# Optimization experiments

Hardware: AMD Instinct MI355X
Metric: run time of the kernel (lower is better)

Reference implementation:

```python
import jax, jax.numpy as jnp
import numpy as np


def setup_inputs() -> dict:
    key = jax.random.key(0)
    k0, k1, k2, k3 = jax.random.split(key, 4)
    B, N, C = 4, 1024, 64
    x = jax.random.normal(k0, (B, N, C), dtype=jnp.float32)
    # torch nn.Linear weights are [out, in]; all projections are bias-free
    W1 = jax.random.normal(k1, (C, C), dtype=jnp.float32) * (1.0 / np.sqrt(C))
    W2 = jax.random.normal(k2, (C, C), dtype=jnp.float32) * (1.0 / np.sqrt(C))
    w3 = jax.random.normal(k3, (C,), dtype=jnp.float32) * (1.0 / np.sqrt(C))
    return {"x": x, "W1": W1, "W2": W2, "w3": w3}


def reference(x, W1, W2, w3):
    # x: [B, N, C]; torch Linear: y = x @ W.T
    x1 = jnp.einsum("bnc,dc->bnd", x, W1)  # [B, N, C]
    x2 = jnp.einsum("bnc,dc->bnd", x, W2)  # [B, N, C]
    # broadcast-add over node pairs, tanh, project C -> 1: [B, N, N]
    combined = jnp.tanh(x1[:, :, None, :] + x2[:, None, :, :])  # [B, N, N, C]
    att = jnp.einsum("bijc,c->bij", combined, w3)
    return jax.nn.softmax(att, axis=-1)
```

## Files before the change

kernel.cpp:

```cpp
#include <hip/hip_runtime.h>
#include <hip/hip_bf16.h>


#define BATCH 4
#define NN    1024
#define CC    64
#define TI    4
#define BLK   256
#define J2    2
#define NCH   (NN / (BLK * J2))
#define PP    65

__device__ __forceinline__ float fast_exp2(float x) {
#if __has_builtin(__builtin_amdgcn_exp2f)
    return __builtin_amdgcn_exp2f(x);
#else
    return exp2f(x);
#endif
}
__device__ __forceinline__ float fast_rcp(float x) {
#if __has_builtin(__builtin_amdgcn_rcpf)
    return __builtin_amdgcn_rcpf(x);
#else
    return 1.0f / x;
#endif
}

__global__ __launch_bounds__(256) void proj_kernel(
    const float* __restrict__ x, const float* __restrict__ W1,
    const float* __restrict__ W2, float* __restrict__ e1p,
    float* __restrict__ e2p) {
    __shared__ float w1t[CC * PP];
    __shared__ float w2t[CC * PP];

    const int tid = threadIdx.x;
    {
        const float4* __restrict__ W1v = (const float4*)W1;
        const float4* __restrict__ W2v = (const float4*)W2;
#pragma unroll
        for (int k = 0; k < 4; ++k) {
            const int fi = k * 256 + tid;
            const int r  = fi >> 4;
            const int c4 = (fi & 15) * 4;
            float4 a = W1v[fi], b = W2v[fi];
            w1t[(c4 + 0) * PP + r] = a.x; w1t[(c4 + 1) * PP + r] = a.y;
            w1t[(c4 + 2) * PP + r] = a.z; w1t[(c4 + 3) * PP + r] = a.w;
            w2t[(c4 + 0) * PP + r] = b.x; w2t[(c4 + 1) * PP + r] = b.y;
            w2t[(c4 + 2) * PP + r] = b.z; w2t[(c4 + 3) * PP + r] = b.w;
        }
    }
    __syncthreads();

    const int w    = tid >> 6;
    const int lane = tid & 63;
    const int r    = blockIdx.x * 4 + w;
    const float4* __restrict__ xr = (const float4*)(x + (size_t)r * CC);

    float a1 = 0.f, a2 = 0.f;
#pragma unroll
    for (int q = 0; q < 16; ++q) {
        const float4 xv = xr[q];
        const float xc[4] = {xv.x, xv.y, xv.z, xv.w};
#pragma unroll
        for (int m = 0; m < 4; ++m) {
            const int c = 4 * q + m;
            a1 = fmaf(xc[m], w1t[c * PP + lane], a1);
            a2 = fmaf(xc[m], w2t[c * PP + lane], a2);
        }
    }
    const float K2 = 2.8853900817779268f;
    e1p[(size_t)r * CC + lane] = fast_exp2(fminf(a1 * K2, 15.f));
    e2p[(size_t)r * CC + lane] = fast_exp2(fminf(a2 * K2, 15.f));
}

__device__ __forceinline__ void step2(float e1a, float e1b, float e2,
                                      float wc, float2& acc) {
    float da = fmaf(e1a, e2, 1.f);
    float db = fmaf(e1b, e2, 1.f);
    float r  = fast_rcp(da * db);
    acc.x = fmaf(wc * db, r, acc.x);
    acc.y = fmaf(wc * da, r, acc.y);
}

__global__ __launch_bounds__(BLK) void attn_kernel(
    const float* __restrict__ e1p, const float* __restrict__ e2p,
    const float* __restrict__ w3, float* __restrict__ out) {
    __shared__ float e1t[CC * TI];
    __shared__ float att_lds[TI * NN];

    const int tid = threadIdx.x;
    const int bi  = blockIdx.x;
    const int b   = bi >> 8;
    const int i0  = (bi & 255) * TI;

    {
        const int ii = tid >> 6, c = tid & 63;
        e1t[c * TI + ii] = e1p[(size_t)((b << 10) + i0 + ii) * CC + c];
    }
    __syncthreads();

    const float4* __restrict__ w3q = (const float4*)w3;
    float sumw3 = 0.f;
#pragma unroll
    for (int q = 0; q < 16; ++q) {
        float4 t = w3q[q];
        sumw3 += (t.x + t.y) + (t.z + t.w);
    }

    const float* __restrict__ e2b = e2p + ((size_t)b << 10) * CC;
    const float4* e1t4 = (const float4*)e1t;

#pragma unroll 1
    for (int ch = 0; ch < NCH; ++ch) {
        const int j0 = ch * (BLK * J2) + tid;
        const float4* __restrict__ rowA = (const float4*)(e2b + (size_t)j0 * CC);
        const float4* __restrict__ rowB = rowA + (BLK * CC / 4);

        float2 accA0 = {0.f, 0.f}, accA1 = {0.f, 0.f};
        float2 accB0 = {0.f, 0.f}, accB1 = {0.f, 0.f};

#pragma unroll 1
        for (int ct = 0; ct < 4; ++ct) {
#pragma unroll
            for (int q = 0; q < 4; ++q) {
                const float4 eAv = rowA[ct * 4 + q];
                const float4 eBv = rowB[ct * 4 + q];
                const float4 wv  = w3q[ct * 4 + q];
                const float eAa[4] = {eAv.x, eAv.y, eAv.z, eAv.w};
                const float eBa[4] = {eBv.x, eBv.y, eBv.z, eBv.w};
                const float wa[4]  = {wv.x, wv.y, wv.z, wv.w};
#pragma unroll
                for (int m = 0; m < 4; ++m) {
                    const int c = ct * 16 + q * 4 + m;
                    const float4 ev = e1t4[c];
                    step2(ev.x, ev.y, eAa[m], wa[m], accA0);
                    step2(ev.z, ev.w, eAa[m], wa[m], accA1);
                    step2(ev.x, ev.y, eBa[m], wa[m], accB0);
                    step2(ev.z, ev.w, eBa[m], wa[m], accB1);
                }
            }
        }
        const int j1 = j0 + BLK;
        att_lds[0 * NN + j0] = fmaf(-2.f, accA0.x, sumw3);
        att_lds[1 * NN + j0] = fmaf(-2.f, accA0.y, sumw3);
        att_lds[2 * NN + j0] = fmaf(-2.f, accA1.x, sumw3);
        att_lds[3 * NN + j0] = fmaf(-2.f, accA1.y, sumw3);
        att_lds[0 * NN + j1] = fmaf(-2.f, accB0.x, sumw3);
        att_lds[1 * NN + j1] = fmaf(-2.f, accB0.y, sumw3);
        att_lds[2 * NN + j1] = fmaf(-2.f, accB1.x, sumw3);
        att_lds[3 * NN + j1] = fmaf(-2.f, accB1.y, sumw3);
    }
    __syncthreads();

    {
        const int w    = tid >> 6;
        const int lane = tid & 63;
        float v[16];
        float m = -3.4e38f;
#pragma unroll
        for (int k = 0; k < 16; ++k) {
            v[k] = att_lds[w * NN + k * 64 + lane];
            m = fmaxf(m, v[k]);
        }
#pragma unroll
        for (int off = 32; off >= 1; off >>= 1)
            m = fmaxf(m, __shfl_xor(m, off));
        const float L2E = 1.4426950408889634f;
        float s = 0.f;
#pragma unroll
        for (int k = 0; k < 16; ++k) {
            v[k] = fast_exp2((v[k] - m) * L2E);
            s += v[k];
        }
#pragma unroll
        for (int off = 32; off >= 1; off >>= 1)
            s += __shfl_xor(s, off);
        const float rs = fast_rcp(s);
        float* __restrict__ orow = out + (((size_t)(b << 10) + (i0 + w)) << 10);
#pragma unroll
        for (int k = 0; k < 16; ++k) orow[k * 64 + lane] = v[k] * rs;
    }
}

extern "C" void kernel_launch(void* const* d_in, const int* in_sizes, int n_in,
                              void* d_out, int out_size, void* d_ws, size_t ws_size,
                              hipStream_t stream) {
    const float* x  = (const float*)d_in[0];
    const float* W1 = (const float*)d_in[1];
    const float* W2 = (const float*)d_in[2];
    const float* w3 = (const float*)d_in[3];
    float* outp = (float*)d_out;

    float* e1p = (float*)d_ws;
    float* e2p = e1p + (size_t)BATCH * NN * CC;

    proj_kernel<<<dim3(BATCH * NN / 4), dim3(256), 0, stream>>>(x, W1, W2, e1p, e2p);
    attn_kernel<<<dim3(BATCH * NN / TI), dim3(BLK), 0, stream>>>(e1p, e2p, w3, outp);
}
```

Before: 104.4 us.

## Halve rows per attention block, batch projection rows, trim step2 multiplies

The attention kernel now processes 2 query rows per block instead of 4, doubling the grid to 2048 blocks so more blocks are available to fill the GPU, at the cost of reloading each e2 row twice as often per query. The projection kernel stages 16 x rows in shared memory and has each wave compute 4 rows, so each W-transposed shared-memory load is reused across rows and fewer blocks redo the weight transpose. step2 factors wc*r into one product, dropping one multiply per pair. During softmax, half the waves in each attention block now sit idle.

```diff
diff --git a/kernel.cpp b/kernel.cpp
--- a/kernel.cpp
+++ b/kernel.cpp
@@ -5,11 +5,12 @@
 #define BATCH 4
 #define NN    1024
 #define CC    64
-#define TI    4
+#define TI    2
 #define BLK   256
 #define J2    2
 #define NCH   (NN / (BLK * J2))
 #define PP    65
+#define PROWS 16
 
 __device__ __forceinline__ float fast_exp2(float x) {
 #if __has_builtin(__builtin_amdgcn_exp2f)
@@ -32,8 +33,10 @@
     float* __restrict__ e2p) {
     __shared__ float w1t[CC * PP];
     __shared__ float w2t[CC * PP];
+    __shared__ float xs[PROWS * CC];
 
     const int tid = threadIdx.x;
+    const int r0  = blockIdx.x * PROWS;
     {
         const float4* __restrict__ W1v = (const float4*)W1;
         const float4* __restrict__ W2v = (const float4*)W2;
@@ -48,29 +51,41 @@
             w2t[(c4 + 0) * PP + r] = b.x; w2t[(c4 + 1) * PP + r] = b.y;
             w2t[(c4 + 2) * PP + r] = b.z; w2t[(c4 + 3) * PP + r] = b.w;
         }
+        const int rr = tid >> 6, c = tid & 63;
+#pragma unroll
+        for (int k = 0; k < 4; ++k) {
+            const int r = k * 4 + rr;
+            xs[r * CC + c] = x[(size_t)(r0 + r) * CC + c];
+        }
     }
     __syncthreads();
 
     const int w    = tid >> 6;
     const int lane = tid & 63;
-    const int r    = blockIdx.x * 4 + w;
-    const float4* __restrict__ xr = (const float4*)(x + (size_t)r * CC);
-
-    float a1 = 0.f, a2 = 0.f;
-#pragma unroll
-    for (int q = 0; q < 16; ++q) {
-        const float4 xv = xr[q];
-        const float xc[4] = {xv.x, xv.y, xv.z, xv.w};
-#pragma unroll
-        for (int m = 0; m < 4; ++m) {
-            const int c = 4 * q + m;
-            a1 = fmaf(xc[m], w1t[c * PP + lane], a1);
-            a2 = fmaf(xc[m], w2t[c * PP + lane], a2);
-        }
+    const int rb   = w * 4;
+
+    float a1[4] = {0.f, 0.f, 0.f, 0.f};
+    float a2[4] = {0.f, 0.f, 0.f, 0.f};
+#pragma unroll
+    for (int c = 0; c < CC; ++c) {
+        const float w1v = w1t[c * PP + lane];
+        const float w2v = w2t[c * PP + lane];
+        const float x0 = xs[(rb + 0) * CC + c];
+        const float x1 = xs[(rb + 1) * CC + c];
+        const float x2v = xs[(rb + 2) * CC + c];
+        const float x3 = xs[(rb + 3) * CC + c];
+        a1[0] = fmaf(x0, w1v, a1[0]);  a2[0] = fmaf(x0, w2v, a2[0]);
+        a1[1] = fmaf(x1, w1v, a1[1]);  a2[1] = fmaf(x1, w2v, a2[1]);
+        a1[2] = fmaf(x2v, w1v, a1[2]); a2[2] = fmaf(x2v, w2v, a2[2]);
+        a1[3] = fmaf(x3, w1v, a1[3]);  a2[3] = fmaf(x3, w2v, a2[3]);
     }
     const float K2 = 2.8853900817779268f;
-    e1p[(size_t)r * CC + lane] = fast_exp2(fminf(a1 * K2, 15.f));
-    e2p[(size_t)r * CC + lane] = fast_exp2(fminf(a2 * K2, 15.f));
+#pragma unroll
+    for (int rr = 0; rr < 4; ++rr) {
+        const size_t r = (size_t)(r0 + rb + rr);
+        e1p[r * CC + lane] = fast_exp2(fminf(a1[rr] * K2, 15.f));
+        e2p[r * CC + lane] = fast_exp2(fminf(a2[rr] * K2, 15.f));
+    }
 }
 
 __device__ __forceinline__ void step2(float e1a, float e1b, float e2,
@@ -78,8 +93,9 @@
     float da = fmaf(e1a, e2, 1.f);
     float db = fmaf(e1b, e2, 1.f);
     float r  = fast_rcp(da * db);
-    acc.x = fmaf(wc * db, r, acc.x);
-    acc.y = fmaf(wc * da, r, acc.y);
+    float t  = wc * r;
+    acc.x = fmaf(db, t, acc.x);
+    acc.y = fmaf(da, t, acc.y);
 }
 
 __global__ __launch_bounds__(BLK) void attn_kernel(
@@ -90,10 +106,10 @@
 
     const int tid = threadIdx.x;
     const int bi  = blockIdx.x;
-    const int b   = bi >> 8;
-    const int i0  = (bi & 255) * TI;
-
-    {
+    const int b   = bi >> 9;
+    const int i0  = (bi & 511) * TI;
+
+    if (tid < CC * TI) {
         const int ii = tid >> 6, c = tid & 63;
         e1t[c * TI + ii] = e1p[(size_t)((b << 10) + i0 + ii) * CC + c];
     }
@@ -108,7 +124,7 @@
     }
 
     const float* __restrict__ e2b = e2p + ((size_t)b << 10) * CC;
-    const float4* e1t4 = (const float4*)e1t;
+    const float2* e1t2 = (const float2*)e1t;
 
 #pragma unroll 1
     for (int ch = 0; ch < NCH; ++ch) {
@@ -116,8 +132,7 @@
         const float4* __restrict__ rowA = (const float4*)(e2b + (size_t)j0 * CC);
         const float4* __restrict__ rowB = rowA + (BLK * CC / 4);
 
-        float2 accA0 = {0.f, 0.f}, accA1 = {0.f, 0.f};
-        float2 accB0 = {0.f, 0.f}, accB1 = {0.f, 0.f};
+        float2 accA = {0.f, 0.f}, accB = {0.f, 0.f};
 
 #pragma unroll 1
         for (int ct = 0; ct < 4; ++ct) {
@@ -132,53 +147,49 @@
 #pragma unroll
                 for (int m = 0; m < 4; ++m) {
                     const int c = ct * 16 + q * 4 + m;
-                    const float4 ev = e1t4[c];
-                    step2(ev.x, ev.y, eAa[m], wa[m], accA0);
-                    step2(ev.z, ev.w, eAa[m], wa[m], accA1);
-                    step2(ev.x, ev.y, eBa[m], wa[m], accB0);
-                    step2(ev.z, ev.w, eBa[m], wa[m], accB1);
+                    const float2 ev = e1t2[c];
+                    step2(ev.x, ev.y, eAa[m], wa[m], accA);
+                    step2(ev.x, ev.y, eBa[m], wa[m], accB);
                 }
             }
         }
         const int j1 = j0 + BLK;
-        att_lds[0 * NN + j0] = fmaf(-2.f, accA0.x, sumw3);
-        att_lds[1 * NN + j0] = fmaf(-2.f, accA0.y, sumw3);
-        att_lds[2 * NN + j0] = fmaf(-2.f, accA1.x, sumw3);
-        att_lds[3 * NN + j0] = fmaf(-2.f, accA1.y, sumw3);
-        att_lds[0 * NN + j1] = fmaf(-2.f, accB0.x, sumw3);
-        att_lds[1 * NN + j1] = fmaf(-2.f, accB0.y, sumw3);
-        att_lds[2 * NN + j1] = fmaf(-2.f, accB1.x, sumw3);
-        att_lds[3 * NN + j1] = fmaf(-2.f, accB1.y, sumw3);
+        att_lds[0 * NN + j0] = fmaf(-2.f, accA.x, sumw3);
+        att_lds[1 * NN + j0] = fmaf(-2.f, accA.y, sumw3);
+        att_lds[0 * NN + j1] = fmaf(-2.f, accB.x, sumw3);
+        att_lds[1 * NN + j1] = fmaf(-2.f, accB.y, sumw3);
     }
     __syncthreads();
 
     {
         const int w    = tid >> 6;
         const int lane = tid & 63;
-        float v[16];
-        float m = -3.4e38f;
-#pragma unroll
-        for (int k = 0; k < 16; ++k) {
-            v[k] = att_lds[w * NN + k * 64 + lane];
-            m = fmaxf(m, v[k]);
-        }
-#pragma unroll
-        for (int off = 32; off >= 1; off >>= 1)
-            m = fmaxf(m, __shfl_xor(m, off));
-        const float L2E = 1.4426950408889634f;
-        float s = 0.f;
-#pragma unroll
-        for (int k = 0; k < 16; ++k) {
-            v[k] = fast_exp2((v[k] - m) * L2E);
-            s += v[k];
-        }
-#pragma unroll
-        for (int off = 32; off >= 1; off >>= 1)
-            s += __shfl_xor(s, off);
-        const float rs = fast_rcp(s);
-        float* __restrict__ orow = out + (((size_t)(b << 10) + (i0 + w)) << 10);
-#pragma unroll
-        for (int k = 0; k < 16; ++k) orow[k * 64 + lane] = v[k] * rs;
+        if (w < TI) {
+            float v[16];
+            float m = -3.4e38f;
+#pragma unroll
+            for (int k = 0; k < 16; ++k) {
+                v[k] = att_lds[w * NN + k * 64 + lane];
+                m = fmaxf(m, v[k]);
+            }
+#pragma unroll
+            for (int off = 32; off >= 1; off >>= 1)
+                m = fmaxf(m, __shfl_xor(m, off));
+            const float L2E = 1.4426950408889634f;
+            float s = 0.f;
+#pragma unroll
+            for (int k = 0; k < 16; ++k) {
+                v[k] = fast_exp2((v[k] - m) * L2E);
+                s += v[k];
+            }
+#pragma unroll
+            for (int off = 32; off >= 1; off >>= 1)
+                s += __shfl_xor(s, off);
+            const float rs = fast_rcp(s);
+            float* __restrict__ orow = out + (((size_t)(b << 10) + (i0 + w)) << 10);
+#pragma unroll
+            for (int k = 0; k < 16; ++k) orow[k * 64 + lane] = v[k] * rs;
+        }
     }
 }
 
@@ -194,6 +205,6 @@
     float* e1p = (float*)d_ws;
     float* e2p = e1p + (size_t)BATCH * NN * CC;
 
-    proj_kernel<<<dim3(BATCH * NN / 4), dim3(256), 0, stream>>>(x, W1, W2, e1p, e2p);
+    proj_kernel<<<dim3(BATCH * NN / PROWS), dim3(256), 0, stream>>>(x, W1, W2, e1p, e2p);
     attn_kernel<<<dim3(BATCH * NN / TI), dim3(BLK), 0, stream>>>(e1p, e2p, w3, outp);
 }
```

New measurement: 130.3 us. 24.8% more time.
